# Kernel tuning notes

Measured on AMD Instinct MI355X. Metric: run time of the kernel, lower is better.

Reference implementation:

```python
import jax, jax.numpy as jnp
import numpy as np

NEG_SLOPE = 0.2


def _gat(x, W, a_src, a_dst, bias, src, dst, nonself, N):
    # PyG GATConv (eval mode): h = x @ W -> [N,H,C]; per-edge scores with
    # LeakyReLU, softmax over incoming edges per target node (self loops
    # re-added after removing any existing ones), weighted scatter-add.
    H, C = a_src.shape
    h = (x @ W).reshape(N, H, C)
    al_s = jnp.einsum('nhc,hc->nh', h, a_src)  # [N,H]
    al_d = jnp.einsum('nhc,hc->nh', h, a_dst)
    e = jax.nn.leaky_relu(al_s[src] + al_d[dst], NEG_SLOPE)  # [E,H]
    e = jnp.where(nonself[:, None], e, -jnp.inf)  # drop input self loops
    e_self = jax.nn.leaky_relu(al_s + al_d, NEG_SLOPE)  # added self loops [N,H]
    m = jnp.maximum(jax.ops.segment_max(e, dst, num_segments=N), e_self)
    w = jnp.exp(e - m[dst])  # masked edges -> 0
    w_self = jnp.exp(e_self - m)
    num = jax.ops.segment_sum(w[:, :, None] * h[src], dst, num_segments=N)
    num = num + w_self[:, :, None] * h
    den = jax.ops.segment_sum(w, dst, num_segments=N) + w_self
    return (num / den[:, :, None]).reshape(N, H * C) + bias


def setup_inputs() -> dict:
    N, E = 100000, 3200000
    key = jax.random.key(0)
    ks = jax.random.split(key, 20)
    s = 0.1
    return {
        'x1': jax.random.normal(ks[0], (N, 7), jnp.float32),
        'x2': jax.random.normal(ks[1], (N, 1), jnp.float32),
        'edge_index': jax.random.randint(ks[2], (2, E), 0, N, jnp.int64)
            if jax.config.jax_enable_x64 else jax.random.randint(ks[2], (2, E), 0, N, jnp.int32),
        'num_nodes': N,
        'lin1_w': s * jax.random.normal(ks[3], (1, 7), jnp.float32),
        'lin1_b': s * jax.random.normal(ks[4], (1,), jnp.float32),
        'lin2_w': s * jax.random.normal(ks[5], (1, 8), jnp.float32),
        'W1': s * jax.random.normal(ks[6], (1, 32), jnp.float32),
        'a_src1': s * jax.random.normal(ks[7], (8, 4), jnp.float32),
        'a_dst1': s * jax.random.normal(ks[8], (8, 4), jnp.float32),
        'b1': s * jax.random.normal(ks[9], (32,), jnp.float32),
        'W2': s * jax.random.normal(ks[10], (32, 16), jnp.float32),
        'a_src2': s * jax.random.normal(ks[11], (4, 4), jnp.float32),
        'a_dst2': s * jax.random.normal(ks[12], (4, 4), jnp.float32),
        'b2': s * jax.random.normal(ks[13], (16,), jnp.float32),
        'W3': s * jax.random.normal(ks[14], (16, 8), jnp.float32),
        'a_src3': s * jax.random.normal(ks[15], (2, 4), jnp.float32),
        'a_dst3': s * jax.random.normal(ks[16], (2, 4), jnp.float32),
        'b3': s * jax.random.normal(ks[17], (8,), jnp.float32),
    }


def reference(x1, x2, edge_index, num_nodes, lin1_w, lin1_b, lin2_w,
              W1, a_src1, a_dst1, b1, W2, a_src2, a_dst2, b2,
              W3, a_src3, a_dst3, b3):
    N = num_nodes
    src, dst = edge_index[0], edge_index[1]
    nonself = src != dst
    # init score + 3 GAT layers (dropouts inactive in eval mode)
    h0 = jax.nn.relu(x1 @ lin1_w.T + lin1_b)  # [N,1]
    x3 = jax.nn.relu(_gat(h0, W1, a_src1, a_dst1, b1, src, dst, nonself, N))
    x4 = jax.nn.relu(_gat(x3, W2, a_src2, a_dst2, b2, src, dst, nonself, N))
    x6 = jax.nn.relu(_gat(x4, W3, a_src3, a_dst3, b3, src, dst, nonself, N))  # [N,8]
    # Row-normalized adjacency with diagonal filled to 1 (sparse form of the
    # original dense Adj): Adj[i,j] = 1/deg[i] on edges (i!=j) and diagonal.
    ns = nonself.astype(x6.dtype)
    deg = 1.0 + jax.ops.segment_sum(ns, src, num_segments=N)  # [N]
    # local score: rowsum(Adj * (x6 x6^T))
    dots = jnp.sum(x6[src] * x6[dst], axis=-1) * ns  # [E]
    local = (jax.ops.segment_sum(dots, src, num_segments=N)
             + jnp.sum(x6 * x6, axis=-1)) / deg  # [N]
    # global score: lin2(Adj @ x6)
    R3 = (jax.ops.segment_sum(x6[dst] * ns[:, None], src, num_segments=N)
          + x6) / deg[:, None]  # [N,8]
    return local[:, None] + R3 @ lin2_w.T  # [N,1]
```

## Files before the change

kernel.cpp:

```cpp
#include <hip/hip_runtime.h>
#include <hip/hip_fp16.h>
#include <math.h>

static constexpr float NEG_SLOPE = 0.2f;
static constexpr int P      = 256;
static constexpr int CAP    = 14000;
static constexpr int CHSZ   = 4096;

__device__ __forceinline__ float lrelu(float x) { return x > 0.0f ? x : NEG_SLOPE * x; }

__device__ __forceinline__ void dm(int x, unsigned int mg, int npr, int& r, int& lk) {
    r = (int)__umulhi((unsigned int)x, mg);
    lk = x - r * npr;
    if (lk >= npr) { lk -= npr; ++r; }
    else if (lk < 0) { lk += npr; --r; }
}

union H8 { int4 i4; __half2 h2[4]; };

__device__ __forceinline__ void h8_to_f(int4 v, float* o) {
    H8 u; u.i4 = v;
#pragma unroll
    for (int k = 0; k < 4; ++k) {
        float2 f = __half22float2(u.h2[k]);
        o[2 * k] = f.x; o[2 * k + 1] = f.y;
    }
}

__device__ __forceinline__ int4 f_to_h8(const float* s) {
    H8 u;
#pragma unroll
    for (int k = 0; k < 4; ++k)
        u.h2[k] = __float22half2_rn(make_float2(s[2 * k], s[2 * k + 1]));
    return u.i4;
}

__global__ __launch_bounds__(512) void part2_kernel(
    const int* __restrict__ src, const int* __restrict__ dst,
    int* __restrict__ gcount,
    unsigned int* __restrict__ stgd, unsigned int* __restrict__ stgs,
    int E, int npr, unsigned int mg)
{
    __shared__ int cntw[8 * P];
    __shared__ int base[P];
    __shared__ int pref[P];
    __shared__ int wsum[8];
    __shared__ unsigned int buf[CHSZ];
    __shared__ unsigned char rid[CHSZ];
    const int dir = blockIdx.x & 1;
    const int c = blockIdx.x >> 1;
    const int i0 = c * CHSZ;
    const int i1 = min(i0 + CHSZ, E);
    const int tot = i1 - i0;
    const int tid = threadIdx.x;
    const int lane = tid & 63, w = tid >> 6;
    const int* key = dir ? (src + i0) : (dst + i0);
    const int* val = dir ? (dst + i0) : (src + i0);
    unsigned int* stg = dir ? stgs : stgd;
    int* gc = gcount + dir * P;
    int* mycnt = cntw + w * P;
    for (int i = tid; i < 8 * P; i += 512) cntw[i] = 0;
    __syncthreads();
    const int nv = tot >> 2;
    const int4* k4 = (const int4*)key;
    for (int t = tid; t < nv; t += 512) {
        int4 k = k4[t];
        int r, lk;
        dm(k.x, mg, npr, r, lk); atomicAdd(&mycnt[r], 1);
        dm(k.y, mg, npr, r, lk); atomicAdd(&mycnt[r], 1);
        dm(k.z, mg, npr, r, lk); atomicAdd(&mycnt[r], 1);
        dm(k.w, mg, npr, r, lk); atomicAdd(&mycnt[r], 1);
    }
    for (int i = (nv << 2) + tid; i < tot; i += 512) {
        int r, lk;
        dm(key[i], mg, npr, r, lk);
        atomicAdd(&mycnt[r], 1);
    }
    __syncthreads();
    int cq[8];
    int tb = 0, x = 0;
    if (tid < P) {
#pragma unroll
        for (int q = 0; q < 8; ++q) { cq[q] = cntw[q * P + tid]; tb += cq[q]; }
        base[tid] = atomicAdd(&gc[tid], tb);
        x = tb;
#pragma unroll
        for (int off = 1; off < 64; off <<= 1) {
            int y = __shfl_up(x, off);
            if (lane >= off) x += y;
        }
        if (lane == 63) wsum[w] = x;
    }
    __syncthreads();
    if (tid < P) {
        int wpref = 0;
#pragma unroll
        for (int k = 0; k < 4; ++k) if (k < w) wpref += wsum[k];
        int ex = x + wpref - tb;
        pref[tid] = ex;
        int acc = ex;
#pragma unroll
        for (int q = 0; q < 8; ++q) { cntw[q * P + tid] = acc; acc += cq[q]; }
    }
    __syncthreads();
    int* mytick = cntw + w * P;
    for (int t = tid; t < nv; t += 512) {
        int4 k = k4[t];
        const int4* v4 = (const int4*)val;
        int4 v = v4[t];
        int r, lk, p;
        dm(k.x, mg, npr, r, lk); p = atomicAdd(&mytick[r], 1);
        buf[p] = ((unsigned int)lk << 17) | (unsigned int)v.x; rid[p] = (unsigned char)r;
        dm(k.y, mg, npr, r, lk); p = atomicAdd(&mytick[r], 1);
        buf[p] = ((unsigned int)lk << 17) | (unsigned int)v.y; rid[p] = (unsigned char)r;
        dm(k.z, mg, npr, r, lk); p = atomicAdd(&mytick[r], 1);
        buf[p] = ((unsigned int)lk << 17) | (unsigned int)v.z; rid[p] = (unsigned char)r;
        dm(k.w, mg, npr, r, lk); p = atomicAdd(&mytick[r], 1);
        buf[p] = ((unsigned int)lk << 17) | (unsigned int)v.w; rid[p] = (unsigned char)r;
    }
    for (int i = (nv << 2) + tid; i < tot; i += 512) {
        int r, lk;
        dm(key[i], mg, npr, r, lk);
        int p = atomicAdd(&mytick[r], 1);
        buf[p] = ((unsigned int)lk << 17) | (unsigned int)val[i];
        rid[p] = (unsigned char)r;
    }
    __syncthreads();
    for (int i = tid; i < tot; i += 512) {
        int r = (int)rid[i];
        int b = base[r] + (i - pref[r]);
        if (b < CAP) stg[(size_t)r * CAP + b] = buf[i];
    }
}

__global__ __launch_bounds__(512) void build_kernel(
    const unsigned int* __restrict__ stgd, const unsigned int* __restrict__ stgs,
    const int* __restrict__ gtot,
    const float* __restrict__ h0, float* __restrict__ colh0,
    int* __restrict__ col_dst, int* __restrict__ col_src,
    int* __restrict__ deg_dst, int* __restrict__ deg_src,
    int* __restrict__ row_dst, int* __restrict__ row_src,
    int N, int npr)
{
    __shared__ int cntw[2 * 512];
    __shared__ int wtmp[8];
    __shared__ int s_eb;
    __shared__ int outv[CAP];
    const int dir = blockIdx.x >> 8;
    const int r = blockIdx.x & (P - 1);
    const unsigned int* stg = (dir ? stgs : stgd) + (size_t)r * CAP;
    int tot = gtot[dir * P + r];
    if (tot > CAP) tot = CAP;
    const int n0 = r * npr;
    const int nb = min(npr, N - n0);
    const int tid = threadIdx.x;
    const int lane = tid & 63, w = tid >> 6;
    const int g = tid >> 8;
    int* mycnt = cntw + g * 512;
    cntw[tid] = 0; cntw[512 + tid] = 0;
    int contrib = (tid < r) ? gtot[dir * P + tid] : 0;
    int rsum = contrib;
#pragma unroll
    for (int off = 1; off < 64; off <<= 1) rsum += __shfl_xor(rsum, off);
    if (lane == 0) wtmp[w] = rsum;
    __syncthreads();
    if (tid == 0) {
        int a = 0;
#pragma unroll
        for (int k = 0; k < 8; ++k) a += wtmp[k];
        s_eb = a;
    }
    __syncthreads();
    const int eb = s_eb;
    for (int i = tid; i < tot; i += 512)
        atomicAdd(&mycnt[stg[i] >> 17], 1);
    __syncthreads();
    int c0 = cntw[tid], c1 = cntw[512 + tid];
    int v = c0 + c1;
    int x = v;
#pragma unroll
    for (int off = 1; off < 64; off <<= 1) {
        int y = __shfl_up(x, off);
        if (lane >= off) x += y;
    }
    if (lane == 63) wtmp[w] = x;
    __syncthreads();
    if (tid == 0) {
        int a = 0;
#pragma unroll
        for (int k = 0; k < 8; ++k) { int t2 = wtmp[k]; wtmp[k] = a; a += t2; }
    }
    __syncthreads();
    int ex = x + wtmp[w] - v;
    if (tid < nb) {
        (dir ? deg_src : deg_dst)[n0 + tid] = v;
        (dir ? row_src : row_dst)[n0 + tid] = eb + ex;
    }
    cntw[tid] = ex;
    cntw[512 + tid] = ex + c0;
    __syncthreads();
    for (int i = tid; i < tot; i += 512) {
        unsigned int wv = stg[i];
        int t = atomicAdd(&mycnt[wv >> 17], 1);
        unsigned int vv = wv & 0x1FFFFu;
        unsigned int self = (vv == (unsigned int)(n0) + (wv >> 17)) ? 0x80000000u : 0u;
        outv[t] = (int)(vv | self);
    }
    __syncthreads();
    if (dir == 0) {
        int* col = col_dst + eb;
        float* ch = colh0 + eb;
        for (int i = tid; i < tot; i += 512) {
            int vv = outv[i];
            col[i] = vv;
            ch[i] = (vv < 0) ? -1.0f : h0[vv];
        }
    } else {
        int* col = col_src + eb;
        for (int i = tid; i < tot; i += 512) col[i] = outv[i];
    }
}

__global__ __launch_bounds__(256) void l1h0_kernel(
    const float* __restrict__ x1, const float* __restrict__ lin1_w,
    const float* __restrict__ lin1_b, float* __restrict__ h0, int N)
{
    int n = blockIdx.x * blockDim.x + threadIdx.x;
    if (n >= N) return;
    float acc = lin1_b[0];
#pragma unroll
    for (int k = 0; k < 7; ++k) acc = fmaf(x1[n * 7 + k], lin1_w[k], acc);
    h0[n] = fmaxf(acc, 0.0f);
}

__global__ __launch_bounds__(256) void gat_gather1_kernel(
    const int* __restrict__ row_start, const int* __restrict__ degv,
    const float* __restrict__ colh0, const float* __restrict__ h0,
    const float* __restrict__ W1, const float* __restrict__ a_src,
    const float* __restrict__ a_dst, const float* __restrict__ bias,
    const float* __restrict__ W2, int4* __restrict__ h2p, int N)
{
    int t = blockIdx.x * 256 + threadIdx.x;
    int n = t >> 3, lane = t & 7;
    if (n >= N) return;
    float cs[8], cd[8];
#pragma unroll
    for (int hd = 0; hd < 8; ++hd) {
        float s = 0.0f, d = 0.0f;
#pragma unroll
        for (int c = 0; c < 4; ++c) {
            s = fmaf(W1[hd * 4 + c], a_src[hd * 4 + c], s);
            d = fmaf(W1[hd * 4 + c], a_dst[hd * 4 + c], d);
        }
        cs[hd] = s; cd[hd] = d;
    }
    float h0n = h0[n];
    float wh[8], den[8], adn[8];
#pragma unroll
    for (int hd = 0; hd < 8; ++hd) {
// ... 41 lines not shown
    for (int m = 1; m < 8; m <<= 1) {
#pragma unroll
        for (int hd = 0; hd < 8; ++hd) {
            den[hd] += __shfl_xor(den[hd], m);
            wh[hd]  += __shfl_xor(wh[hd], m);
        }
    }
    float fct = wh[lane] / den[lane];
    const float4 wv = ((const float4*)W1)[lane];
    const float4 bb = ((const float4*)bias)[lane];
    float xr[4];
    xr[0] = fmaxf(fmaf(fct, wv.x, bb.x), 0.0f);
    xr[1] = fmaxf(fmaf(fct, wv.y, bb.y), 0.0f);
    xr[2] = fmaxf(fmaf(fct, wv.z, bb.z), 0.0f);
    xr[3] = fmaxf(fmaf(fct, wv.w, bb.w), 0.0f);
    float pj[16];
#pragma unroll
    for (int j = 0; j < 16; ++j) pj[j] = 0.0f;
    const float* wbase = W2 + lane * 64;
#pragma unroll
    for (int c2 = 0; c2 < 4; ++c2) {
#pragma unroll
        for (int j = 0; j < 16; ++j)
            pj[j] = fmaf(xr[c2], wbase[c2 * 16 + j], pj[j]);
    }
#pragma unroll
    for (int m = 1; m < 8; m <<= 1) {
#pragma unroll
        for (int j = 0; j < 16; ++j) pj[j] += __shfl_xor(pj[j], m);
    }
    if (lane < 2) h2p[(size_t)n * 2 + lane] = f_to_h8(pj + lane * 8);
}

__device__ __forceinline__ void g2_acc(
    const float* hs, const float* As, const float* ald, float* num, float* den)
{
#pragma unroll
    for (int hd = 0; hd < 4; ++hd) {
        float a = 0.0f;
#pragma unroll
        for (int c = 0; c < 4; ++c) a = fmaf(hs[hd * 4 + c], As[hd * 4 + c], a);
        float w = __expf(lrelu(a + ald[hd]));
        den[hd] += w;
#pragma unroll
        for (int c = 0; c < 4; ++c) num[hd * 4 + c] = fmaf(w, hs[hd * 4 + c], num[hd * 4 + c]);
    }
}

__global__ __launch_bounds__(256) void gat_gather2_kernel(
    const int* __restrict__ row_start, const int* __restrict__ degv,
    const int* __restrict__ col, const int4* __restrict__ hp,
    const float* __restrict__ a_src, const float* __restrict__ a_dst,
    const float* __restrict__ bias, const float* __restrict__ W3,
    int4* __restrict__ h3p, int N)
{
    int t = blockIdx.x * 256 + threadIdx.x;
    int n = t >> 3, lane = t & 7;
    if (n >= N) return;
    float As[16], Ad[16];
#pragma unroll
    for (int j = 0; j < 16; ++j) { As[j] = a_src[j]; Ad[j] = a_dst[j]; }
    float hn[16];
    h8_to_f(hp[(size_t)n * 2], hn);
    h8_to_f(hp[(size_t)n * 2 + 1], hn + 8);
    float ald[4];
#pragma unroll
    for (int hd = 0; hd < 4; ++hd) {
        float d = 0.0f;
#pragma unroll
        for (int c = 0; c < 4; ++c) d = fmaf(hn[hd * 4 + c], Ad[hd * 4 + c], d);
        ald[hd] = d;
    }
    float num[16], den[4];
    if (lane == 0) {
#pragma unroll
        for (int hd = 0; hd < 4; ++hd) {
            float a = 0.0f;
#pragma unroll
            for (int c = 0; c < 4; ++c) a = fmaf(hn[hd * 4 + c], As[hd * 4 + c], a);
            float w = __expf(lrelu(a + ald[hd]));
            den[hd] = w;
#pragma unroll
            for (int c = 0; c < 4; ++c) num[hd * 4 + c] = w * hn[hd * 4 + c];
        }
    } else {
#pragma unroll
        for (int j = 0; j < 16; ++j) num[j] = 0.0f;
#pragma unroll
        for (int hd = 0; hd < 4; ++hd) den[hd] = 0.0f;
    }
    int start = row_start[n];
    int end = start + degv[n];
    int e = start + lane;
    for (; e + 8 < end; e += 16) {
        int s0 = col[e], s1 = col[e + 8];
        int i0 = s0 & 0x7fffffff, i1 = s1 & 0x7fffffff;
        int4 q00 = hp[(size_t)i0 * 2], q01 = hp[(size_t)i0 * 2 + 1];
        int4 q10 = hp[(size_t)i1 * 2], q11 = hp[(size_t)i1 * 2 + 1];
        if (s0 >= 0) {
            float hs[16];
            h8_to_f(q00, hs); h8_to_f(q01, hs + 8);
            g2_acc(hs, As, ald, num, den);
        }
        if (s1 >= 0) {
            float hs[16];
            h8_to_f(q10, hs); h8_to_f(q11, hs + 8);
            g2_acc(hs, As, ald, num, den);
        }
    }
    if (e < end) {
        int s0 = col[e];
        if (s0 >= 0) {
            float hs[16];
            h8_to_f(hp[(size_t)(s0 & 0x7fffffff) * 2], hs);
            h8_to_f(hp[(size_t)(s0 & 0x7fffffff) * 2 + 1], hs + 8);
            g2_acc(hs, As, ald, num, den);
        }
    }
#pragma unroll
    for (int m = 1; m < 8; m <<= 1) {
#pragma unroll
        for (int hd = 0; hd < 4; ++hd) den[hd] += __shfl_xor(den[hd], m);
#pragma unroll
        for (int j = 0; j < 16; ++j) num[j] += __shfl_xor(num[j], m);
    }
    float invd[4];
#pragma unroll
    for (int hd = 0; hd < 4; ++hd) invd[hd] = 1.0f / den[hd];
    float pj[8];
#pragma unroll
    for (int j = 0; j < 8; ++j) pj[j] = 0.0f;
#pragma unroll
    for (int k = 0; k < 16; ++k) {
        float xk = fmaxf(fmaf(num[k], invd[k >> 2], bias[k]), 0.0f);
        const float* wrow = W3 + k * 8;
#pragma unroll
        for (int j = 0; j < 8; ++j) pj[j] = fmaf(xk, wrow[j], pj[j]);
    }
    if (lane == 0) h3p[n] = f_to_h8(pj);
}

__device__ __forceinline__ void g3_acc(
    const float* hs, const float* As, const float* ald, float* num, float* den)
{
#pragma unroll
    for (int hd = 0; hd < 2; ++hd) {
        float a = 0.0f;
#pragma unroll
        for (int c = 0; c < 4; ++c) a = fmaf(hs[hd * 4 + c], As[hd * 4 + c], a);
        float w = __expf(lrelu(a + ald[hd]));
        den[hd] += w;
#pragma unroll
        for (int c = 0; c < 4; ++c) num[hd * 4 + c] = fmaf(w, hs[hd * 4 + c], num[hd * 4 + c]);
    }
}

__global__ __launch_bounds__(256) void gat_gather3_kernel(
    const int* __restrict__ row_start, const int* __restrict__ degv,
    const int* __restrict__ col, const int4* __restrict__ hp,
    const float* __restrict__ a_src, const float* __restrict__ a_dst,
    const float* __restrict__ bias, int4* __restrict__ x6p, int N)
{
    int t = blockIdx.x * 256 + threadIdx.x;
    int n = t >> 3, lane = t & 7;
    if (n >= N) return;
    float As[8], Ad[8];
#pragma unroll
    for (int j = 0; j < 8; ++j) { As[j] = a_src[j]; Ad[j] = a_dst[j]; }
    float hn[8];
    h8_to_f(hp[n], hn);
    float ald[2];
#pragma unroll
    for (int hd = 0; hd < 2; ++hd) {
        float d = 0.0f;
#pragma unroll
        for (int c = 0; c < 4; ++c) d = fmaf(hn[hd * 4 + c], Ad[hd * 4 + c], d);
        ald[hd] = d;
    }
    float num[8], den[2];
    if (lane == 0) {
#pragma unroll
        for (int hd = 0; hd < 2; ++hd) {
            float a = 0.0f;
#pragma unroll
            for (int c = 0; c < 4; ++c) a = fmaf(hn[hd * 4 + c], As[hd * 4 + c], a);
            float w = __expf(lrelu(a + ald[hd]));
            den[hd] = w;
#pragma unroll
            for (int c = 0; c < 4; ++c) num[hd * 4 + c] = w * hn[hd * 4 + c];
        }
    } else {
#pragma unroll
        for (int j = 0; j < 8; ++j) num[j] = 0.0f;
        den[0] = den[1] = 0.0f;
    }
    int start = row_start[n];
    int end = start + degv[n];
    int e = start + lane;
    for (; e + 8 < end; e += 16) {
        int s0 = col[e], s1 = col[e + 8];
        int i0 = s0 & 0x7fffffff, i1 = s1 & 0x7fffffff;
        int4 q0 = hp[i0], q1 = hp[i1];
        if (s0 >= 0) {
            float hs[8];
            h8_to_f(q0, hs);
            g3_acc(hs, As, ald, num, den);
        }
        if (s1 >= 0) {
            float hs[8];
            h8_to_f(q1, hs);
            g3_acc(hs, As, ald, num, den);
        }
    }
    if (e < end) {
        int s0 = col[e];
        if (s0 >= 0) {
            float hs[8];
            h8_to_f(hp[s0 & 0x7fffffff], hs);
            g3_acc(hs, As, ald, num, den);
        }
    }
#pragma unroll
    for (int m = 1; m < 8; m <<= 1) {
        den[0] += __shfl_xor(den[0], m);
        den[1] += __shfl_xor(den[1], m);
#pragma unroll
        for (int j = 0; j < 8; ++j) num[j] += __shfl_xor(num[j], m);
    }
    if (lane == 0) {
        float o[8];
        float i0 = 1.0f / den[0], i1 = 1.0f / den[1];
#pragma unroll
        for (int c = 0; c < 4; ++c) {
            o[c]     = fmaxf(fmaf(num[c], i0, bias[c]), 0.0f);
            o[4 + c] = fmaxf(fmaf(num[4 + c], i1, bias[4 + c]), 0.0f);
        }
        x6p[n] = f_to_h8(o);
    }
}

__global__ __launch_bounds__(256) void score_gather_kernel(
    const int* __restrict__ row_start, const int* __restrict__ degv,
    const int* __restrict__ col, const int4* __restrict__ x6p,
    const float* __restrict__ lin2_w, float* __restrict__ out, int N)
{
    int t = blockIdx.x * 256 + threadIdx.x;
    int n = t >> 3, lane = t & 7;
    if (n >= N) return;
    float sx[8];
    h8_to_f(x6p[n], sx);
    float r[8];
    int sc = 0;
    if (lane == 0) {
#pragma unroll
        for (int j = 0; j < 8; ++j) r[j] = sx[j];
    } else {
#pragma unroll
        for (int j = 0; j < 8; ++j) r[j] = 0.0f;
    }
    int start = row_start[n];
    int dg = degv[n];
    int end = start + dg;
    int e = start + lane;
    for (; e + 8 < end; e += 16) {
        int d0 = col[e], d1 = col[e + 8];
        int i0 = d0 & 0x7fffffff, i1 = d1 & 0x7fffffff;
        int4 q0 = x6p[i0], q1 = x6p[i1];
        if (d0 < 0) { ++sc; }
        else {
            float dx[8];
            h8_to_f(q0, dx);
#pragma unroll
            for (int j = 0; j < 8; ++j) r[j] += dx[j];
        }
        if (d1 < 0) { ++sc; }
        else {
            float dx[8];
            h8_to_f(q1, dx);
#pragma unroll
            for (int j = 0; j < 8; ++j) r[j] += dx[j];
        }
    }
    if (e < end) {
        int d0 = col[e];
        if (d0 < 0) { ++sc; }
        else {
            float dx[8];
            h8_to_f(x6p[d0 & 0x7fffffff], dx);
#pragma unroll
            for (int j = 0; j < 8; ++j) r[j] += dx[j];
        }
    }
#pragma unroll
    for (int m = 1; m < 8; m <<= 1) {
        sc += __shfl_xor(sc, m);
#pragma unroll
        for (int j = 0; j < 8; ++j) r[j] += __shfl_xor(r[j], m);
    }
    if (lane == 0) {
        float invd = 1.0f / (1.0f + (float)(dg - sc));
        float loc = 0.0f, g = 0.0f;
#pragma unroll
        for (int j = 0; j < 8; ++j) {
            loc = fmaf(sx[j], r[j], loc);
            g   = fmaf(r[j], lin2_w[j], g);
        }
        out[n] = (loc + g) * invd;
    }
}

extern "C" void kernel_launch(void* const* d_in, const int* in_sizes, int n_in,
                              void* d_out, int out_size, void* d_ws, size_t ws_size,
                              hipStream_t stream)
{
    const float* x1     = (const float*)d_in[0];
    const int*   ei     = (const int*)d_in[2];
    const float* lin1_w = (const float*)d_in[4];
    const float* lin1_b = (const float*)d_in[5];
    const float* lin2_w = (const float*)d_in[6];
    const float* W1     = (const float*)d_in[7];
    const float* a_src1 = (const float*)d_in[8];
    const float* a_dst1 = (const float*)d_in[9];
    const float* b1     = (const float*)d_in[10];
    const float* W2     = (const float*)d_in[11];
    const float* a_src2 = (const float*)d_in[12];
    const float* a_dst2 = (const float*)d_in[13];
    const float* b2     = (const float*)d_in[14];
    const float* W3     = (const float*)d_in[15];
    const float* a_src3 = (const float*)d_in[16];
    const float* a_dst3 = (const float*)d_in[17];
    const float* b3     = (const float*)d_in[18];
    float* out = (float*)d_out;

    const int N = in_sizes[0] / 7;
    const int E = in_sizes[2] / 2;
    const int* src = ei;
    const int* dst = ei + E;

    const int npr = (N + P - 1) / P;
    const unsigned int mg = (unsigned int)((0x100000000ULL + npr - 1) / (unsigned long long)npr);
    const int PB = (E + CHSZ - 1) / CHSZ;

    size_t Ns = (size_t)N, Es = (size_t)E;
    int* ideg_dst = (int*)d_ws;
    int* ideg_src = ideg_dst + Ns;
    int* irow_dst = ideg_src + Ns;
    int* irow_src = irow_dst + Ns;
    int* gcount   = irow_src + Ns;
    int* icol_dst = gcount + 2 * P;
    int* icol_src = icol_dst + Es;
    float* f = (float*)(icol_src + Es);
    unsigned int* stgd = (unsigned int*)f;
    unsigned int* stgs = stgd + (size_t)P * CAP;
    float* h0    = f + 72 * Ns;
    float* colh0 = f + 73 * Ns;
    int4*  h2p   = (int4*)f;
    int4*  h3p   = (int4*)(f + 8 * Ns);
    int4*  x6p   = (int4*)(f + 12 * Ns);

    const int TB = 256;
    const int gN  = (N + TB - 1) / TB;
    const int g8  = (8 * N + TB - 1) / TB;

    l1h0_kernel<<<gN, TB, 0, stream>>>(x1, lin1_w, lin1_b, h0, N);

    hipMemsetAsync(gcount, 0, 2 * P * sizeof(int), stream);
    part2_kernel<<<2 * PB, 512, 0, stream>>>(src, dst, gcount, stgd, stgs, E, npr, mg);
    build_kernel<<<2 * P, 512, 0, stream>>>(stgd, stgs, gcount, h0, colh0,
                                            icol_dst, icol_src,
                                            ideg_dst, ideg_src,
                                            irow_dst, irow_src, N, npr);

    gat_gather1_kernel<<<g8, TB, 0, stream>>>(irow_dst, ideg_dst, colh0,
                                              h0, W1, a_src1, a_dst1, b1, W2, h2p, N);

    gat_gather2_kernel<<<g8, TB, 0, stream>>>(irow_dst, ideg_dst, icol_dst,
                                              h2p, a_src2, a_dst2, b2, W3, h3p, N);

    gat_gather3_kernel<<<g8, TB, 0, stream>>>(irow_dst, ideg_dst, icol_dst,
                                              h3p, a_src3, a_dst3, b3, x6p, N);

    score_gather_kernel<<<g8, TB, 0, stream>>>(irow_src, ideg_src, icol_src,
                                               x6p, lin2_w, out, N);
}
```

Before: 261.9 us.

## Score directly from staged src partitions with LDS atomics, drop src CSR build

Removes the src-direction CSR construction in build_kernel and replaces the per-node score gather with a per-partition kernel that reads staged (local key, dst) words and accumulates neighbor features with shared-memory atomics. It also folds the gcount memset into the first kernel and parallelizes the W3 projection across the 8 lanes in gather2. This saves a sort/scatter pass and a memset launch, but the new score kernel runs only 256 blocks and performs many LDS float atomics per edge, which may limit parallelism.

```diff
diff --git a/kernel.cpp b/kernel.cpp
--- a/kernel.cpp
+++ b/kernel.cpp
@@ -134,22 +134,18 @@
 }
 
 __global__ __launch_bounds__(512) void build_kernel(
-    const unsigned int* __restrict__ stgd, const unsigned int* __restrict__ stgs,
-    const int* __restrict__ gtot,
+    const unsigned int* __restrict__ stgd, const int* __restrict__ gtot,
     const float* __restrict__ h0, float* __restrict__ colh0,
-    int* __restrict__ col_dst, int* __restrict__ col_src,
-    int* __restrict__ deg_dst, int* __restrict__ deg_src,
-    int* __restrict__ row_dst, int* __restrict__ row_src,
-    int N, int npr)
+    int* __restrict__ col_dst, int* __restrict__ deg_dst,
+    int* __restrict__ row_dst, int N, int npr)
 {
     __shared__ int cntw[2 * 512];
     __shared__ int wtmp[8];
     __shared__ int s_eb;
     __shared__ int outv[CAP];
-    const int dir = blockIdx.x >> 8;
-    const int r = blockIdx.x & (P - 1);
-    const unsigned int* stg = (dir ? stgs : stgd) + (size_t)r * CAP;
-    int tot = gtot[dir * P + r];
+    const int r = blockIdx.x;
+    const unsigned int* stg = stgd + (size_t)r * CAP;
+    int tot = gtot[r];
     if (tot > CAP) tot = CAP;
     const int n0 = r * npr;
     const int nb = min(npr, N - n0);
@@ -158,7 +154,7 @@
     const int g = tid >> 8;
     int* mycnt = cntw + g * 512;
     cntw[tid] = 0; cntw[512 + tid] = 0;
-    int contrib = (tid < r) ? gtot[dir * P + tid] : 0;
+    int contrib = (tid < r) ? gtot[tid] : 0;
     int rsum = contrib;
 #pragma unroll
     for (int off = 1; off < 64; off <<= 1) rsum += __shfl_xor(rsum, off);
@@ -193,8 +189,8 @@
     __syncthreads();
     int ex = x + wtmp[w] - v;
     if (tid < nb) {
-        (dir ? deg_src : deg_dst)[n0 + tid] = v;
-        (dir ? row_src : row_dst)[n0 + tid] = eb + ex;
+        deg_dst[n0 + tid] = v;
+        row_dst[n0 + tid] = eb + ex;
     }
     cntw[tid] = ex;
     cntw[512 + tid] = ex + c0;
@@ -207,24 +203,24 @@
         outv[t] = (int)(vv | self);
     }
     __syncthreads();
-    if (dir == 0) {
-        int* col = col_dst + eb;
-        float* ch = colh0 + eb;
-        for (int i = tid; i < tot; i += 512) {
-            int vv = outv[i];
-            col[i] = vv;
-            ch[i] = (vv < 0) ? -1.0f : h0[vv];
-        }
-    } else {
-        int* col = col_src + eb;
-        for (int i = tid; i < tot; i += 512) col[i] = outv[i];
+    int* col = col_dst + eb;
+    float* ch = colh0 + eb;
+    for (int i = tid; i < tot; i += 512) {
+        int vv = outv[i];
+        col[i] = vv;
+        ch[i] = (vv < 0) ? -1.0f : h0[vv];
     }
 }
 
 __global__ __launch_bounds__(256) void l1h0_kernel(
     const float* __restrict__ x1, const float* __restrict__ lin1_w,
-    const float* __restrict__ lin1_b, float* __restrict__ h0, int N)
-{
+    const float* __restrict__ lin1_b, int* __restrict__ gcount,
+    float* __restrict__ h0, int N)
+{
+    if (blockIdx.x == 0) {
+        gcount[threadIdx.x] = 0;
+        gcount[256 + threadIdx.x] = 0;
+    }
     int n = blockIdx.x * blockDim.x + threadIdx.x;
     if (n >= N) return;
     float acc = lin1_b[0];
@@ -352,7 +348,7 @@
     const int* __restrict__ col, const int4* __restrict__ hp,
     const float* __restrict__ a_src, const float* __restrict__ a_dst,
     const float* __restrict__ bias, const float* __restrict__ W3,
-    int4* __restrict__ h3p, int N)
+    __half* __restrict__ h3h, int N)
 {
     int t = blockIdx.x * 256 + threadIdx.x;
     int n = t >> 3, lane = t & 7;
@@ -427,17 +423,13 @@
     float invd[4];
 #pragma unroll
     for (int hd = 0; hd < 4; ++hd) invd[hd] = 1.0f / den[hd];
-    float pj[8];
-#pragma unroll
-    for (int j = 0; j < 8; ++j) pj[j] = 0.0f;
+    float pj = 0.0f;
 #pragma unroll
     for (int k = 0; k < 16; ++k) {
         float xk = fmaxf(fmaf(num[k], invd[k >> 2], bias[k]), 0.0f);
-        const float* wrow = W3 + k * 8;
-#pragma unroll
-        for (int j = 0; j < 8; ++j) pj[j] = fmaf(xk, wrow[j], pj[j]);
-    }
-    if (lane == 0) h3p[n] = f_to_h8(pj);
+        pj = fmaf(xk, W3[k * 8 + lane], pj);
+    }
+    h3h[(size_t)n * 8 + lane] = __float2half_rn(pj);
 }
 
 __device__ __forceinline__ void g3_acc(
@@ -539,73 +531,69 @@
     }
 }
 
-__global__ __launch_bounds__(256) void score_gather_kernel(
-    const int* __restrict__ row_start, const int* __restrict__ degv,
-    const int* __restrict__ col, const int4* __restrict__ x6p,
-    const float* __restrict__ lin2_w, float* __restrict__ out, int N)
-{
-    int t = blockIdx.x * 256 + threadIdx.x;
-    int n = t >> 3, lane = t & 7;
-    if (n >= N) return;
-    float sx[8];
-    h8_to_f(x6p[n], sx);
-    float r[8];
-    int sc = 0;
-    if (lane == 0) {
-#pragma unroll
-        for (int j = 0; j < 8; ++j) r[j] = sx[j];
-    } else {
-#pragma unroll
-        for (int j = 0; j < 8; ++j) r[j] = 0.0f;
-    }
-    int start = row_start[n];
-    int dg = degv[n];
-    int end = start + dg;
-    int e = start + lane;
-    for (; e + 8 < end; e += 16) {
-        int d0 = col[e], d1 = col[e + 8];
-        int i0 = d0 & 0x7fffffff, i1 = d1 & 0x7fffffff;
-        int4 q0 = x6p[i0], q1 = x6p[i1];
-        if (d0 < 0) { ++sc; }
-        else {
+__global__ __launch_bounds__(512) void score_range_kernel(
+    const unsigned int* __restrict__ stgs, const int* __restrict__ gtot,
+    const int4* __restrict__ x6p, const float* __restrict__ lin2_w,
+    float* __restrict__ out, int N, int npr)
+{
+    __shared__ float accs[8][512];
+    __shared__ int cnt[512];
+    const int r = blockIdx.x;
+    const unsigned int* stg = stgs + (size_t)r * CAP;
+    int tot = gtot[P + r];
+    if (tot > CAP) tot = CAP;
+    const int n0 = r * npr;
+    const int nb = min(npr, N - n0);
+    const int tid = threadIdx.x;
+#pragma unroll
+    for (int j = 0; j < 8; ++j) accs[j][tid] = 0.0f;
+    cnt[tid] = 0;
+    __syncthreads();
+    int i = tid;
+    for (; i + 512 < tot; i += 1024) {
+        unsigned int w0 = stg[i], w1 = stg[i + 512];
+        int lk0 = (int)(w0 >> 17), d0 = (int)(w0 & 0x1FFFFu);
+        int lk1 = (int)(w1 >> 17), d1 = (int)(w1 & 0x1FFFFu);
+        int4 q0 = x6p[d0], q1 = x6p[d1];
+        if (d0 != n0 + lk0) {
             float dx[8];
             h8_to_f(q0, dx);
 #pragma unroll
-            for (int j = 0; j < 8; ++j) r[j] += dx[j];
-        }
-        if (d1 < 0) { ++sc; }
-        else {
+            for (int j = 0; j < 8; ++j) atomicAdd(&accs[j][lk0], dx[j]);
+            atomicAdd(&cnt[lk0], 1);
+        }
+        if (d1 != n0 + lk1) {
             float dx[8];
             h8_to_f(q1, dx);
 #pragma unroll
-            for (int j = 0; j < 8; ++j) r[j] += dx[j];
-        }
-    }
-    if (e < end) {
-        int d0 = col[e];
-        if (d0 < 0) { ++sc; }
-        else {
+            for (int j = 0; j < 8; ++j) atomicAdd(&accs[j][lk1], dx[j]);
+            atomicAdd(&cnt[lk1], 1);
+        }
+    }
+    if (i < tot) {
+        unsigned int w0 = stg[i];
+        int lk0 = (int)(w0 >> 17), d0 = (int)(w0 & 0x1FFFFu);
+        if (d0 != n0 + lk0) {
             float dx[8];
-            h8_to_f(x6p[d0 & 0x7fffffff], dx);
-#pragma unroll
-            for (int j = 0; j < 8; ++j) r[j] += dx[j];
-        }
-    }
-#pragma unroll
-    for (int m = 1; m < 8; m <<= 1) {
-        sc += __shfl_xor(sc, m);
-#pragma unroll
-        for (int j = 0; j < 8; ++j) r[j] += __shfl_xor(r[j], m);
-    }
-    if (lane == 0) {
-        float invd = 1.0f / (1.0f + (float)(dg - sc));
+            h8_to_f(x6p[d0], dx);
+#pragma unroll
+            for (int j = 0; j < 8; ++j) atomicAdd(&accs[j][lk0], dx[j]);
+            atomicAdd(&cnt[lk0], 1);
+        }
+    }
+    __syncthreads();
+    for (int lk = tid; lk < nb; lk += 512) {
+        float sx[8];
+        h8_to_f(x6p[n0 + lk], sx);
+        float invd = 1.0f / (1.0f + (float)cnt[lk]);
         float loc = 0.0f, g = 0.0f;
 #pragma unroll
         for (int j = 0; j < 8; ++j) {
-            loc = fmaf(sx[j], r[j], loc);
-            g   = fmaf(r[j], lin2_w[j], g);
-        }
-        out[n] = (loc + g) * invd;
+            float rj = accs[j][lk] + sx[j];
+            loc = fmaf(sx[j], rj, loc);
+            g   = fmaf(rj, lin2_w[j], g);
+        }
+        out[n0 + lk] = (loc + g) * invd;
     }
 }
 
@@ -643,13 +631,10 @@
 
     size_t Ns = (size_t)N, Es = (size_t)E;
     int* ideg_dst = (int*)d_ws;
-    int* ideg_src = ideg_dst + Ns;
-    int* irow_dst = ideg_src + Ns;
-    int* irow_src = irow_dst + Ns;
-    int* gcount   = irow_src + Ns;
+    int* irow_dst = ideg_dst + Ns;
+    int* gcount   = irow_dst + Ns;
     int* icol_dst = gcount + 2 * P;
-    int* icol_src = icol_dst + Es;
-    float* f = (float*)(icol_src + Es);
+    float* f = (float*)(icol_dst + Es);
     unsigned int* stgd = (unsigned int*)f;
     unsigned int* stgs = stgd + (size_t)P * CAP;
     float* h0    = f + 72 * Ns;
@@ -662,24 +647,22 @@
     const int gN  = (N + TB - 1) / TB;
     const int g8  = (8 * N + TB - 1) / TB;
 
-    l1h0_kernel<<<gN, TB, 0, stream>>>(x1, lin1_w, lin1_b, h0, N);
-
-    hipMemsetAsync(gcount, 0, 2 * P * sizeof(int), stream);
+    l1h0_kernel<<<gN, TB, 0, stream>>>(x1, lin1_w, lin1_b, gcount, h0, N);
+
     part2_kernel<<<2 * PB, 512, 0, stream>>>(src, dst, gcount, stgd, stgs, E, npr, mg);
-    build_kernel<<<2 * P, 512, 0, stream>>>(stgd, stgs, gcount, h0, colh0,
-                                            icol_dst, icol_src,
-                                            ideg_dst, ideg_src,
-                                            irow_dst, irow_src, N, npr);
+    build_kernel<<<P, 512, 0, stream>>>(stgd, gcount, h0, colh0,
+                                        icol_dst, ideg_dst, irow_dst, N, npr);
 
     gat_gather1_kernel<<<g8, TB, 0, stream>>>(irow_dst, ideg_dst, colh0,
                                               h0, W1, a_src1, a_dst1, b1, W2, h2p, N);
 
     gat_gather2_kernel<<<g8, TB, 0, stream>>>(irow_dst, ideg_dst, icol_dst,
-                                              h2p, a_src2, a_dst2, b2, W3, h3p, N);
+                                              h2p, a_src2, a_dst2, b2, W3,
+                                              (__half*)h3p, N);
 
     gat_gather3_kernel<<<g8, TB, 0, stream>>>(irow_dst, ideg_dst, icol_dst,
                                               h3p, a_src3, a_dst3, b3, x6p, N);
 
-    score_gather_kernel<<<g8, TB, 0, stream>>>(irow_src, ideg_src, icol_src,
-                                               x6p, lin2_w, out, N);
-}
+    score_range_kernel<<<P, 512, 0, stream>>>(stgs, gcount, x6p, lin2_w,
+                                              out, N, npr);
+}
```

Result: slower. 370.2 us (+41.3%).

## Split GAT layers 2 and 3 gathers across heads with 32 lanes per node

Applied to the files above, without the earlier changes.

Gather kernels for GAT layers 2 and 3 now use 32 threads per node instead of 8. Lanes are split into head × edge-group, so each thread loads only its head's 4 fp16 features (an int2) per neighbor rather than the whole row. This raises parallelism and memory-level concurrency on the irregular gathers, but issues more, smaller loads and adds cross-lane shuffles for the W3 projection. It also folds the gcount memset into the first elementwise kernel to remove a separate launch.

```diff
diff --git a/kernel.cpp b/kernel.cpp
--- a/kernel.cpp
+++ b/kernel.cpp
@@ -33,6 +33,12 @@
     for (int k = 0; k < 4; ++k)
         u.h2[k] = __float22half2_rn(make_float2(s[2 * k], s[2 * k + 1]));
     return u.i4;
+}
+
+__device__ __forceinline__ void i2_to_f(int2 v, float* o) {
+    float2 f0 = __half22float2(*(__half2*)&v.x);
+    float2 f1 = __half22float2(*(__half2*)&v.y);
+    o[0] = f0.x; o[1] = f0.y; o[2] = f1.x; o[3] = f1.y;
 }
 
 __global__ __launch_bounds__(512) void part2_kernel(
@@ -223,8 +229,13 @@
 
 __global__ __launch_bounds__(256) void l1h0_kernel(
     const float* __restrict__ x1, const float* __restrict__ lin1_w,
-    const float* __restrict__ lin1_b, float* __restrict__ h0, int N)
-{
+    const float* __restrict__ lin1_b, int* __restrict__ gcount,
+    float* __restrict__ h0, int N)
+{
+    if (blockIdx.x == 0) {
+        gcount[threadIdx.x] = 0;
+        gcount[256 + threadIdx.x] = 0;
+    }
     int n = blockIdx.x * blockDim.x + threadIdx.x;
     if (n >= N) return;
     float acc = lin1_b[0];
@@ -332,210 +343,153 @@
     if (lane < 2) h2p[(size_t)n * 2 + lane] = f_to_h8(pj + lane * 8);
 }
 
-__device__ __forceinline__ void g2_acc(
-    const float* hs, const float* As, const float* ald, float* num, float* den)
-{
-#pragma unroll
-    for (int hd = 0; hd < 4; ++hd) {
-        float a = 0.0f;
-#pragma unroll
-        for (int c = 0; c < 4; ++c) a = fmaf(hs[hd * 4 + c], As[hd * 4 + c], a);
-        float w = __expf(lrelu(a + ald[hd]));
-        den[hd] += w;
-#pragma unroll
-        for (int c = 0; c < 4; ++c) num[hd * 4 + c] = fmaf(w, hs[hd * 4 + c], num[hd * 4 + c]);
-    }
+__device__ __forceinline__ void g2h_acc(
+    int2 q, const float* As, float ald, float* num, float& den)
+{
+    float hs[4];
+    i2_to_f(q, hs);
+    float a = 0.0f;
+#pragma unroll
+    for (int c = 0; c < 4; ++c) a = fmaf(hs[c], As[c], a);
+    float w = __expf(lrelu(a + ald));
+    den += w;
+#pragma unroll
+    for (int c = 0; c < 4; ++c) num[c] = fmaf(w, hs[c], num[c]);
 }
 
 __global__ __launch_bounds__(256) void gat_gather2_kernel(
     const int* __restrict__ row_start, const int* __restrict__ degv,
-    const int* __restrict__ col, const int4* __restrict__ hp,
+    const int* __restrict__ col, const int2* __restrict__ hp2,
     const float* __restrict__ a_src, const float* __restrict__ a_dst,
     const float* __restrict__ bias, const float* __restrict__ W3,
-    int4* __restrict__ h3p, int N)
+    __half* __restrict__ h3h, int N)
 {
     int t = blockIdx.x * 256 + threadIdx.x;
-    int n = t >> 3, lane = t & 7;
+    int n = t >> 5;
     if (n >= N) return;
-    float As[16], Ad[16];
-#pragma unroll
-    for (int j = 0; j < 16; ++j) { As[j] = a_src[j]; Ad[j] = a_dst[j]; }
-    float hn[16];
-    h8_to_f(hp[(size_t)n * 2], hn);
-    h8_to_f(hp[(size_t)n * 2 + 1], hn + 8);
-    float ald[4];
-#pragma unroll
-    for (int hd = 0; hd < 4; ++hd) {
-        float d = 0.0f;
-#pragma unroll
-        for (int c = 0; c < 4; ++c) d = fmaf(hn[hd * 4 + c], Ad[hd * 4 + c], d);
-        ald[hd] = d;
-    }
-    float num[16], den[4];
-    if (lane == 0) {
-#pragma unroll
-        for (int hd = 0; hd < 4; ++hd) {
-            float a = 0.0f;
-#pragma unroll
-            for (int c = 0; c < 4; ++c) a = fmaf(hn[hd * 4 + c], As[hd * 4 + c], a);
-            float w = __expf(lrelu(a + ald[hd]));
-            den[hd] = w;
-#pragma unroll
-            for (int c = 0; c < 4; ++c) num[hd * 4 + c] = w * hn[hd * 4 + c];
-        }
-    } else {
-#pragma unroll
-        for (int j = 0; j < 16; ++j) num[j] = 0.0f;
-#pragma unroll
-        for (int hd = 0; hd < 4; ++hd) den[hd] = 0.0f;
+    const int wl = threadIdx.x & 63;
+    const int lane = t & 31;
+    const int hd = lane & 3, eg = lane >> 2;
+    float As[4], Ad[4];
+#pragma unroll
+    for (int c = 0; c < 4; ++c) { As[c] = a_src[hd * 4 + c]; Ad[c] = a_dst[hd * 4 + c]; }
+    float hn[4];
+    i2_to_f(hp2[(size_t)n * 4 + hd], hn);
+    float ald = 0.0f;
+#pragma unroll
+    for (int c = 0; c < 4; ++c) ald = fmaf(hn[c], Ad[c], ald);
+    float num[4] = {0.0f, 0.0f, 0.0f, 0.0f};
+    float den = 0.0f;
+    if (eg == 0) {
+        float a = 0.0f;
+#pragma unroll
+        for (int c = 0; c < 4; ++c) a = fmaf(hn[c], As[c], a);
+        float w = __expf(lrelu(a + ald));
+        den = w;
+#pragma unroll
+        for (int c = 0; c < 4; ++c) num[c] = w * hn[c];
     }
     int start = row_start[n];
     int end = start + degv[n];
-    int e = start + lane;
+    int e = start + eg;
     for (; e + 8 < end; e += 16) {
         int s0 = col[e], s1 = col[e + 8];
-        int i0 = s0 & 0x7fffffff, i1 = s1 & 0x7fffffff;
-        int4 q00 = hp[(size_t)i0 * 2], q01 = hp[(size_t)i0 * 2 + 1];
-        int4 q10 = hp[(size_t)i1 * 2], q11 = hp[(size_t)i1 * 2 + 1];
-        if (s0 >= 0) {
-            float hs[16];
-            h8_to_f(q00, hs); h8_to_f(q01, hs + 8);
-            g2_acc(hs, As, ald, num, den);
-        }
-        if (s1 >= 0) {
-            float hs[16];
-            h8_to_f(q10, hs); h8_to_f(q11, hs + 8);
-            g2_acc(hs, As, ald, num, den);
-        }
+        int2 q0 = hp2[(size_t)(s0 & 0x7fffffff) * 4 + hd];
+        int2 q1 = hp2[(size_t)(s1 & 0x7fffffff) * 4 + hd];
+        if (s0 >= 0) g2h_acc(q0, As, ald, num, den);
+        if (s1 >= 0) g2h_acc(q1, As, ald, num, den);
     }
     if (e < end) {
         int s0 = col[e];
-        if (s0 >= 0) {
-            float hs[16];
-            h8_to_f(hp[(size_t)(s0 & 0x7fffffff) * 2], hs);
-            h8_to_f(hp[(size_t)(s0 & 0x7fffffff) * 2 + 1], hs + 8);
-            g2_acc(hs, As, ald, num, den);
-        }
-    }
-#pragma unroll
-    for (int m = 1; m < 8; m <<= 1) {
-#pragma unroll
-        for (int hd = 0; hd < 4; ++hd) den[hd] += __shfl_xor(den[hd], m);
-#pragma unroll
-        for (int j = 0; j < 16; ++j) num[j] += __shfl_xor(num[j], m);
-    }
-    float invd[4];
-#pragma unroll
-    for (int hd = 0; hd < 4; ++hd) invd[hd] = 1.0f / den[hd];
-    float pj[8];
-#pragma unroll
-    for (int j = 0; j < 8; ++j) pj[j] = 0.0f;
-#pragma unroll
-    for (int k = 0; k < 16; ++k) {
-        float xk = fmaxf(fmaf(num[k], invd[k >> 2], bias[k]), 0.0f);
-        const float* wrow = W3 + k * 8;
-#pragma unroll
-        for (int j = 0; j < 8; ++j) pj[j] = fmaf(xk, wrow[j], pj[j]);
-    }
-    if (lane == 0) h3p[n] = f_to_h8(pj);
-}
-
-__device__ __forceinline__ void g3_acc(
-    const float* hs, const float* As, const float* ald, float* num, float* den)
-{
-#pragma unroll
-    for (int hd = 0; hd < 2; ++hd) {
-        float a = 0.0f;
-#pragma unroll
-        for (int c = 0; c < 4; ++c) a = fmaf(hs[hd * 4 + c], As[hd * 4 + c], a);
-        float w = __expf(lrelu(a + ald[hd]));
-        den[hd] += w;
-#pragma unroll
-        for (int c = 0; c < 4; ++c) num[hd * 4 + c] = fmaf(w, hs[hd * 4 + c], num[hd * 4 + c]);
-    }
+        if (s0 >= 0) g2h_acc(hp2[(size_t)(s0 & 0x7fffffff) * 4 + hd], As, ald, num, den);
+    }
+#pragma unroll
+    for (int m = 4; m < 32; m <<= 1) {
+        den += __shfl_xor(den, m);
+#pragma unroll
+        for (int c = 0; c < 4; ++c) num[c] += __shfl_xor(num[c], m);
+    }
+    float invd = 1.0f / den;
+    float x4c[4];
+#pragma unroll
+    for (int c = 0; c < 4; ++c)
+        x4c[c] = fmaxf(fmaf(num[c], invd, bias[hd * 4 + c]), 0.0f);
+    const int j = lane & 7;
+    float pj = 0.0f;
+#pragma unroll
+    for (int hh = 0; hh < 4; ++hh) {
+        int srcl = (wl & ~3) | hh;
+#pragma unroll
+        for (int c = 0; c < 4; ++c) {
+            float xk = __shfl(x4c[c], srcl);
+            pj = fmaf(xk, W3[(hh * 4 + c) * 8 + j], pj);
+        }
+    }
+    if (lane < 8) h3h[(size_t)n * 8 + lane] = __float2half_rn(pj);
 }
 
 __global__ __launch_bounds__(256) void gat_gather3_kernel(
     const int* __restrict__ row_start, const int* __restrict__ degv,
-    const int* __restrict__ col, const int4* __restrict__ hp,
+    const int* __restrict__ col, const int2* __restrict__ hp2,
     const float* __restrict__ a_src, const float* __restrict__ a_dst,
     const float* __restrict__ bias, int4* __restrict__ x6p, int N)
 {
     int t = blockIdx.x * 256 + threadIdx.x;
-    int n = t >> 3, lane = t & 7;
+    int n = t >> 5;
     if (n >= N) return;
-    float As[8], Ad[8];
-#pragma unroll
-    for (int j = 0; j < 8; ++j) { As[j] = a_src[j]; Ad[j] = a_dst[j]; }
-    float hn[8];
-    h8_to_f(hp[n], hn);
-    float ald[2];
-#pragma unroll
-    for (int hd = 0; hd < 2; ++hd) {
-        float d = 0.0f;
-#pragma unroll
-        for (int c = 0; c < 4; ++c) d = fmaf(hn[hd * 4 + c], Ad[hd * 4 + c], d);
-        ald[hd] = d;
-    }
-    float num[8], den[2];
-    if (lane == 0) {
-#pragma unroll
-        for (int hd = 0; hd < 2; ++hd) {
-            float a = 0.0f;
-#pragma unroll
-            for (int c = 0; c < 4; ++c) a = fmaf(hn[hd * 4 + c], As[hd * 4 + c], a);
-            float w = __expf(lrelu(a + ald[hd]));
-            den[hd] = w;
-#pragma unroll
-            for (int c = 0; c < 4; ++c) num[hd * 4 + c] = w * hn[hd * 4 + c];
-        }
-    } else {
-#pragma unroll
-        for (int j = 0; j < 8; ++j) num[j] = 0.0f;
-        den[0] = den[1] = 0.0f;
+    const int lane = t & 31;
+    const int hd = lane & 1, eg = lane >> 1;
+    float As[4], Ad[4];
+#pragma unroll
+    for (int c = 0; c < 4; ++c) { As[c] = a_src[hd * 4 + c]; Ad[c] = a_dst[hd * 4 + c]; }
+    float hn[4];
+    i2_to_f(hp2[(size_t)n * 2 + hd], hn);
+    float ald = 0.0f;
+#pragma unroll
+    for (int c = 0; c < 4; ++c) ald = fmaf(hn[c], Ad[c], ald);
+    float num[4] = {0.0f, 0.0f, 0.0f, 0.0f};
+    float den = 0.0f;
+    if (eg == 0) {
+        float a = 0.0f;
+#pragma unroll
+        for (int c = 0; c < 4; ++c) a = fmaf(hn[c], As[c], a);
+        float w = __expf(lrelu(a + ald));
+        den = w;
+#pragma unroll
+        for (int c = 0; c < 4; ++c) num[c] = w * hn[c];
     }
     int start = row_start[n];
     int end = start + degv[n];
-    int e = start + lane;
-    for (; e + 8 < end; e += 16) {
-        int s0 = col[e], s1 = col[e + 8];
-        int i0 = s0 & 0x7fffffff, i1 = s1 & 0x7fffffff;
-        int4 q0 = hp[i0], q1 = hp[i1];
-        if (s0 >= 0) {
-            float hs[8];
-            h8_to_f(q0, hs);
-            g3_acc(hs, As, ald, num, den);
-        }
-        if (s1 >= 0) {
-            float hs[8];
-            h8_to_f(q1, hs);
-            g3_acc(hs, As, ald, num, den);
-        }
+    int e = start + eg;
+    for (; e + 16 < end; e += 32) {
+        int s0 = col[e], s1 = col[e + 16];
+        int2 q0 = hp2[(size_t)(s0 & 0x7fffffff) * 2 + hd];
+        int2 q1 = hp2[(size_t)(s1 & 0x7fffffff) * 2 + hd];
+        if (s0 >= 0) g2h_acc(q0, As, ald, num, den);
+        if (s1 >= 0) g2h_acc(q1, As, ald, num, den);
     }
     if (e < end) {
         int s0 = col[e];
-        if (s0 >= 0) {
-            float hs[8];
-            h8_to_f(hp[s0 & 0x7fffffff], hs);
-            g3_acc(hs, As, ald, num, den);
-        }
-    }
-#pragma unroll
-    for (int m = 1; m < 8; m <<= 1) {
-        den[0] += __shfl_xor(den[0], m);
-        den[1] += __shfl_xor(den[1], m);
-#pragma unroll
-        for (int j = 0; j < 8; ++j) num[j] += __shfl_xor(num[j], m);
-    }
+        if (s0 >= 0) g2h_acc(hp2[(size_t)(s0 & 0x7fffffff) * 2 + hd], As, ald, num, den);
+    }
+#pragma unroll
+    for (int m = 2; m < 32; m <<= 1) {
+        den += __shfl_xor(den, m);
+#pragma unroll
+        for (int c = 0; c < 4; ++c) num[c] += __shfl_xor(num[c], m);
+    }
+    float invd = 1.0f / den;
+    float o0 = fmaxf(fmaf(num[0], invd, bias[hd * 4 + 0]), 0.0f);
+    float o1 = fmaxf(fmaf(num[1], invd, bias[hd * 4 + 1]), 0.0f);
+    float o2 = fmaxf(fmaf(num[2], invd, bias[hd * 4 + 2]), 0.0f);
+    float o3 = fmaxf(fmaf(num[3], invd, bias[hd * 4 + 3]), 0.0f);
+    __half2 hw0 = __float22half2_rn(make_float2(o0, o1));
+    __half2 hw1 = __float22half2_rn(make_float2(o2, o3));
+    int u0 = *(int*)&hw0, u1 = *(int*)&hw1;
+    int v0 = __shfl_xor(u0, 1), v1 = __shfl_xor(u1, 1);
     if (lane == 0) {
-        float o[8];
-        float i0 = 1.0f / den[0], i1 = 1.0f / den[1];
-#pragma unroll
-        for (int c = 0; c < 4; ++c) {
-            o[c]     = fmaxf(fmaf(num[c], i0, bias[c]), 0.0f);
-            o[4 + c] = fmaxf(fmaf(num[4 + c], i1, bias[4 + c]), 0.0f);
-        }
-        x6p[n] = f_to_h8(o);
+        int4 wv; wv.x = u0; wv.y = u1; wv.z = v0; wv.w = v1;
+        x6p[n] = wv;
     }
 }
 
@@ -564,8 +518,7 @@
     int e = start + lane;
     for (; e + 8 < end; e += 16) {
         int d0 = col[e], d1 = col[e + 8];
-        int i0 = d0 & 0x7fffffff, i1 = d1 & 0x7fffffff;
-        int4 q0 = x6p[i0], q1 = x6p[i1];
+        int4 q0 = x6p[d0 & 0x7fffffff], q1 = x6p[d1 & 0x7fffffff];
         if (d0 < 0) { ++sc; }
         else {
             float dx[8];
@@ -661,10 +614,10 @@
     const int TB = 256;
     const int gN  = (N + TB - 1) / TB;
     const int g8  = (8 * N + TB - 1) / TB;
-
-    l1h0_kernel<<<gN, TB, 0, stream>>>(x1, lin1_w, lin1_b, h0, N);
-
-    hipMemsetAsync(gcount, 0, 2 * P * sizeof(int), stream);
+    const int g32 = (32 * N + TB - 1) / TB;
+
+    l1h0_kernel<<<gN, TB, 0, stream>>>(x1, lin1_w, lin1_b, gcount, h0, N);
+
     part2_kernel<<<2 * PB, 512, 0, stream>>>(src, dst, gcount, stgd, stgs, E, npr, mg);
     build_kernel<<<2 * P, 512, 0, stream>>>(stgd, stgs, gcount, h0, colh0,
                                             icol_dst, icol_src,
@@ -674,11 +627,13 @@
     gat_gather1_kernel<<<g8, TB, 0, stream>>>(irow_dst, ideg_dst, colh0,
                                               h0, W1, a_src1, a_dst1, b1, W2, h2p, N);
 
-    gat_gather2_kernel<<<g8, TB, 0, stream>>>(irow_dst, ideg_dst, icol_dst,
-                                              h2p, a_src2, a_dst2, b2, W3, h3p, N);
-
-    gat_gather3_kernel<<<g8, TB, 0, stream>>>(irow_dst, ideg_dst, icol_dst,
-                                              h3p, a_src3, a_dst3, b3, x6p, N);
+    gat_gather2_kernel<<<g32, TB, 0, stream>>>(irow_dst, ideg_dst, icol_dst,
+                                               (const int2*)h2p, a_src2, a_dst2,
+                                               b2, W3, (__half*)h3p, N);
+
+    gat_gather3_kernel<<<g32, TB, 0, stream>>>(irow_dst, ideg_dst, icol_dst,
+                                               (const int2*)h3p, a_src3, a_dst3,
+                                               b3, x6p, N);
 
     score_gather_kernel<<<g8, TB, 0, stream>>>(irow_src, ideg_src, icol_src,
                                                x6p, lin2_w, out, N);
```

Measured after the change: 274.4 us. +4.8%, slower.

## Double CSR-build partitions to 512 and fold gcount reset into first kernel

Applied to the files above, without the earlier changes.

Raises the number of node partitions used by the two-pass edge bucketing from 256 to 512 and halves the per-partition staging capacity, so build_kernel launches twice as many blocks, each handling about 196 nodes with less shared memory. The partition id array grows to 16-bit, and the scan in part2 now covers all 512 threads. The separate memset of the global counters is replaced by zeroing inside l1h0_kernel, and the colh0 gather loop is unrolled by two. More partitions mean more global atomics and scattered staging writes. The smaller CAP also raises the risk of dropping edges if a partition overflows.

```diff
diff --git a/kernel.cpp b/kernel.cpp
--- a/kernel.cpp
+++ b/kernel.cpp
@@ -3,9 +3,9 @@
 #include <math.h>
 
 static constexpr float NEG_SLOPE = 0.2f;
-static constexpr int P      = 256;
-static constexpr int CAP    = 14000;
-static constexpr int CHSZ   = 4096;
+static constexpr int P    = 512;
+static constexpr int CAP  = 7000;
+static constexpr int CHSZ = 4096;
 
 __device__ __forceinline__ float lrelu(float x) { return x > 0.0f ? x : NEG_SLOPE * x; }
 
@@ -46,7 +46,7 @@
     __shared__ int pref[P];
     __shared__ int wsum[8];
     __shared__ unsigned int buf[CHSZ];
-    __shared__ unsigned char rid[CHSZ];
+    __shared__ unsigned short rid[CHSZ];
     const int dir = blockIdx.x & 1;
     const int c = blockIdx.x >> 1;
     const int i0 = c * CHSZ;
@@ -79,23 +79,21 @@
     __syncthreads();
     int cq[8];
     int tb = 0, x = 0;
-    if (tid < P) {
-#pragma unroll
-        for (int q = 0; q < 8; ++q) { cq[q] = cntw[q * P + tid]; tb += cq[q]; }
-        base[tid] = atomicAdd(&gc[tid], tb);
-        x = tb;
-#pragma unroll
-        for (int off = 1; off < 64; off <<= 1) {
-            int y = __shfl_up(x, off);
-            if (lane >= off) x += y;
-        }
-        if (lane == 63) wsum[w] = x;
-    }
-    __syncthreads();
-    if (tid < P) {
+#pragma unroll
+    for (int q = 0; q < 8; ++q) { cq[q] = cntw[q * P + tid]; tb += cq[q]; }
+    base[tid] = atomicAdd(&gc[tid], tb);
+    x = tb;
+#pragma unroll
+    for (int off = 1; off < 64; off <<= 1) {
+        int y = __shfl_up(x, off);
+        if (lane >= off) x += y;
+    }
+    if (lane == 63) wsum[w] = x;
+    __syncthreads();
+    {
         int wpref = 0;
 #pragma unroll
-        for (int k = 0; k < 4; ++k) if (k < w) wpref += wsum[k];
+        for (int k = 0; k < 8; ++k) if (k < w) wpref += wsum[k];
         int ex = x + wpref - tb;
         pref[tid] = ex;
         int acc = ex;
@@ -110,20 +108,20 @@
         int4 v = v4[t];
         int r, lk, p;
         dm(k.x, mg, npr, r, lk); p = atomicAdd(&mytick[r], 1);
-        buf[p] = ((unsigned int)lk << 17) | (unsigned int)v.x; rid[p] = (unsigned char)r;
+        buf[p] = ((unsigned int)lk << 17) | (unsigned int)v.x; rid[p] = (unsigned short)r;
         dm(k.y, mg, npr, r, lk); p = atomicAdd(&mytick[r], 1);
-        buf[p] = ((unsigned int)lk << 17) | (unsigned int)v.y; rid[p] = (unsigned char)r;
+        buf[p] = ((unsigned int)lk << 17) | (unsigned int)v.y; rid[p] = (unsigned short)r;
         dm(k.z, mg, npr, r, lk); p = atomicAdd(&mytick[r], 1);
-        buf[p] = ((unsigned int)lk << 17) | (unsigned int)v.z; rid[p] = (unsigned char)r;
+        buf[p] = ((unsigned int)lk << 17) | (unsigned int)v.z; rid[p] = (unsigned short)r;
         dm(k.w, mg, npr, r, lk); p = atomicAdd(&mytick[r], 1);
-        buf[p] = ((unsigned int)lk << 17) | (unsigned int)v.w; rid[p] = (unsigned char)r;
+        buf[p] = ((unsigned int)lk << 17) | (unsigned int)v.w; rid[p] = (unsigned short)r;
     }
     for (int i = (nv << 2) + tid; i < tot; i += 512) {
         int r, lk;
         dm(key[i], mg, npr, r, lk);
         int p = atomicAdd(&mytick[r], 1);
         buf[p] = ((unsigned int)lk << 17) | (unsigned int)val[i];
-        rid[p] = (unsigned char)r;
+        rid[p] = (unsigned short)r;
     }
     __syncthreads();
     for (int i = tid; i < tot; i += 512) {
@@ -142,11 +140,11 @@
     int* __restrict__ row_dst, int* __restrict__ row_src,
     int N, int npr)
 {
-    __shared__ int cntw[2 * 512];
+    __shared__ int cntw[2 * 256];
     __shared__ int wtmp[8];
     __shared__ int s_eb;
     __shared__ int outv[CAP];
-    const int dir = blockIdx.x >> 8;
+    const int dir = blockIdx.x >> 9;
     const int r = blockIdx.x & (P - 1);
     const unsigned int* stg = (dir ? stgs : stgd) + (size_t)r * CAP;
     int tot = gtot[dir * P + r];
@@ -156,8 +154,8 @@
     const int tid = threadIdx.x;
     const int lane = tid & 63, w = tid >> 6;
     const int g = tid >> 8;
-    int* mycnt = cntw + g * 512;
-    cntw[tid] = 0; cntw[512 + tid] = 0;
+    int* mycnt = cntw + g * 256;
+    if (tid < 256) { cntw[tid] = 0; cntw[256 + tid] = 0; }
     int contrib = (tid < r) ? gtot[dir * P + tid] : 0;
     int rsum = contrib;
 #pragma unroll
@@ -175,29 +173,31 @@
     for (int i = tid; i < tot; i += 512)
         atomicAdd(&mycnt[stg[i] >> 17], 1);
     __syncthreads();
-    int c0 = cntw[tid], c1 = cntw[512 + tid];
-    int v = c0 + c1;
+    int c0 = 0, c1 = 0, v = 0;
+    if (tid < 256) { c0 = cntw[tid]; c1 = cntw[256 + tid]; v = c0 + c1; }
     int x = v;
 #pragma unroll
     for (int off = 1; off < 64; off <<= 1) {
         int y = __shfl_up(x, off);
         if (lane >= off) x += y;
     }
-    if (lane == 63) wtmp[w] = x;
+    if (tid < 256 && lane == 63) wtmp[w] = x;
     __syncthreads();
     if (tid == 0) {
         int a = 0;
 #pragma unroll
-        for (int k = 0; k < 8; ++k) { int t2 = wtmp[k]; wtmp[k] = a; a += t2; }
-    }
-    __syncthreads();
-    int ex = x + wtmp[w] - v;
-    if (tid < nb) {
-        (dir ? deg_src : deg_dst)[n0 + tid] = v;
-        (dir ? row_src : row_dst)[n0 + tid] = eb + ex;
-    }
-    cntw[tid] = ex;
-    cntw[512 + tid] = ex + c0;
+        for (int k = 0; k < 4; ++k) { int t2 = wtmp[k]; wtmp[k] = a; a += t2; }
+    }
+    __syncthreads();
+    if (tid < 256) {
+        int ex = x + wtmp[w] - v;
+        if (tid < nb) {
+            (dir ? deg_src : deg_dst)[n0 + tid] = v;
+            (dir ? row_src : row_dst)[n0 + tid] = eb + ex;
+        }
+        cntw[tid] = ex;
+        cntw[256 + tid] = ex + c0;
+    }
     __syncthreads();
     for (int i = tid; i < tot; i += 512) {
         unsigned int wv = stg[i];
@@ -210,10 +210,18 @@
     if (dir == 0) {
         int* col = col_dst + eb;
         float* ch = colh0 + eb;
-        for (int i = tid; i < tot; i += 512) {
-            int vv = outv[i];
-            col[i] = vv;
-            ch[i] = (vv < 0) ? -1.0f : h0[vv];
+        int i = tid;
+        for (; i + 512 < tot; i += 1024) {
+            int v0 = outv[i], v1 = outv[i + 512];
+            float a0 = (v0 < 0) ? -1.0f : h0[v0];
+            float a1 = (v1 < 0) ? -1.0f : h0[v1];
+            col[i] = v0; ch[i] = a0;
+            col[i + 512] = v1; ch[i + 512] = a1;
+        }
+        if (i < tot) {
+            int v0 = outv[i];
+            col[i] = v0;
+            ch[i] = (v0 < 0) ? -1.0f : h0[v0];
         }
     } else {
         int* col = col_src + eb;
@@ -223,8 +231,13 @@
 
 __global__ __launch_bounds__(256) void l1h0_kernel(
     const float* __restrict__ x1, const float* __restrict__ lin1_w,
-    const float* __restrict__ lin1_b, float* __restrict__ h0, int N)
-{
+    const float* __restrict__ lin1_b, int* __restrict__ gcount,
+    float* __restrict__ h0, int N)
+{
+    if (blockIdx.x == 0) {
+#pragma unroll
+        for (int q = 0; q < 4; ++q) gcount[q * 256 + threadIdx.x] = 0;
+    }
     int n = blockIdx.x * blockDim.x + threadIdx.x;
     if (n >= N) return;
     float acc = lin1_b[0];
@@ -564,8 +577,7 @@
     int e = start + lane;
     for (; e + 8 < end; e += 16) {
         int d0 = col[e], d1 = col[e + 8];
-        int i0 = d0 & 0x7fffffff, i1 = d1 & 0x7fffffff;
-        int4 q0 = x6p[i0], q1 = x6p[i1];
+        int4 q0 = x6p[d0 & 0x7fffffff], q1 = x6p[d1 & 0x7fffffff];
         if (d0 < 0) { ++sc; }
         else {
             float dx[8];
@@ -662,9 +674,8 @@
     const int gN  = (N + TB - 1) / TB;
     const int g8  = (8 * N + TB - 1) / TB;
 
-    l1h0_kernel<<<gN, TB, 0, stream>>>(x1, lin1_w, lin1_b, h0, N);
-
-    hipMemsetAsync(gcount, 0, 2 * P * sizeof(int), stream);
+    l1h0_kernel<<<gN, TB, 0, stream>>>(x1, lin1_w, lin1_b, gcount, h0, N);
+
     part2_kernel<<<2 * PB, 512, 0, stream>>>(src, dst, gcount, stgd, stgs, E, npr, mg);
     build_kernel<<<2 * P, 512, 0, stream>>>(stgd, stgs, gcount, h0, colh0,
                                             icol_dst, icol_src,
```

Result: no change. 259.4 us (-1.0%).
